# Kernel tuning notes

Measured on AMD Instinct MI355X. Metric: run time of the kernel, lower is better.

Reference implementation:

```python
import jax, jax.numpy as jnp
import numpy as np

B = 16          # graphs in batch
N = 10000       # original-graph nodes per graph
EG = 20000      # line-graph nodes (edges) per graph
E = B * EG      # total line-graph nodes
D = 384         # dim_inner
H = D // 3      # hdim
TOTAL_NODES = B * N


def setup_inputs() -> dict:
    key = jax.random.key(0)
    k1, k2 = jax.random.split(key)
    x = jax.random.normal(k1, (E, D), dtype=jnp.float32)
    org_graph_size = jnp.full((B,), N, dtype=jnp.int32)
    ptr = jnp.arange(B + 1, dtype=jnp.int32) * EG
    lg_node_idx = jax.random.randint(k2, (E, 2), 0, N, dtype=jnp.int32)
    return {"x": x, "org_graph_size": org_graph_size, "ptr": ptr, "lg_node_idx": lg_node_idx}


def _scatter_mean(x, idx, num_segments):
    # segment mean: sum / count (count clamped to 1 for empty segments)
    s = jax.ops.segment_sum(x, idx, num_segments=num_segments)
    c = jax.ops.segment_sum(jnp.ones((x.shape[0],), x.dtype), idx, num_segments=num_segments)
    return s / jnp.maximum(c, 1.0)[:, None]


def reference(x, org_graph_size, ptr, lg_node_idx):
    # per-graph node-index offsets (cumsum with leading zero, drop last)
    offsets = jnp.cumsum(
        jnp.concatenate([jnp.zeros((1,), org_graph_size.dtype), org_graph_size])
    )[:-1]
    # repeat each graph's offset for each of its line-graph nodes
    edge_counts = ptr[1:] - ptr[:-1]
    padding = jnp.repeat(offsets, edge_counts, total_repeat_length=E)
    idx = lg_node_idx + padding[:, None]  # [E, 2] global node indices

    outgoing = _scatter_mean(x, idx[:, 0], TOTAL_NODES)
    incoming = _scatter_mean(x, idx[:, 1], TOTAL_NODES)

    # lgvariant == 21
    return jnp.concatenate([incoming[:, : 2 * H], outgoing[:, 2 * H :]], axis=1)
```

## Files before the change

kernel.cpp:

```cpp
#include <hip/hip_runtime.h>

#define DIM 384
#define HALFC 256
#define C4PER 96

#define SCAN_BLOCK 256
#define SCAN_ITEMS 8
#define SCAN_CHUNK (SCAN_BLOCK * SCAN_ITEMS)

__global__ void count_kernel(const int* __restrict__ org, const int* __restrict__ ptr,
                             const int* __restrict__ lg, int B, int E, int TN,
                             int* __restrict__ cnt) {
    int e = blockIdx.x * blockDim.x + threadIdx.x;
    if (e >= E) return;
    int off = 0;
    for (int j = 0; j < B; ++j)
        if (e >= ptr[j + 1]) off += org[j];
    int n_out = lg[2 * e]     + off;
    int n_in  = lg[2 * e + 1] + off;
    atomicAdd(&cnt[n_in], 1);
    atomicAdd(&cnt[TN + n_out], 1);
}

__global__ void scan1_kernel(const int* __restrict__ cnt, int* __restrict__ offs,
                             int* __restrict__ bsum, int n) {
    __shared__ int s[SCAN_BLOCK];
    int base = blockIdx.x * SCAN_CHUNK;
    int tid = threadIdx.x;
    int v[SCAN_ITEMS];
    int tsum = 0;
#pragma unroll
    for (int j = 0; j < SCAN_ITEMS; ++j) {
        int i = base + tid * SCAN_ITEMS + j;
        v[j] = (i < n) ? cnt[i] : 0;
        tsum += v[j];
    }
    s[tid] = tsum;
    __syncthreads();
    for (int d = 1; d < SCAN_BLOCK; d <<= 1) {
        int t = (tid >= d) ? s[tid - d] : 0;
        __syncthreads();
        s[tid] += t;
        __syncthreads();
    }
    if (tid == SCAN_BLOCK - 1) bsum[blockIdx.x] = s[SCAN_BLOCK - 1];
    int run = (tid > 0) ? s[tid - 1] : 0;
#pragma unroll
    for (int j = 0; j < SCAN_ITEMS; ++j) {
        int i = base + tid * SCAN_ITEMS + j;
        if (i < n) offs[i] = run;
        run += v[j];
    }
}

__global__ void scan2_kernel(int* __restrict__ bsum, int nb) {
    __shared__ int s[SCAN_BLOCK];
    int tid = threadIdx.x;
    int carry = 0;
    for (int base = 0; base < nb; base += SCAN_BLOCK) {
        int i = base + tid;
        s[tid] = (i < nb) ? bsum[i] : 0;
        __syncthreads();
        for (int d = 1; d < SCAN_BLOCK; d <<= 1) {
            int t = (tid >= d) ? s[tid - d] : 0;
            __syncthreads();
            s[tid] += t;
            __syncthreads();
        }
        int excl = carry + ((tid > 0) ? s[tid - 1] : 0);
        if (i < nb) bsum[i] = excl;
        carry += s[SCAN_BLOCK - 1];
        __syncthreads();
    }
}

__global__ void scan3_kernel(int* __restrict__ offs, const int* __restrict__ bsum, int n) {
    int i = blockIdx.x * blockDim.x + threadIdx.x;
    if (i < n) offs[i] += bsum[i / SCAN_CHUNK];
}

__global__ void fill_kernel(const int* __restrict__ org, const int* __restrict__ ptr,
                            const int* __restrict__ lg, int B, int E, int TN,
                            int* __restrict__ offs, int* __restrict__ list) {
    int e = blockIdx.x * blockDim.x + threadIdx.x;
    if (e >= E) return;
    int off = 0;
    for (int j = 0; j < B; ++j)
        if (e >= ptr[j + 1]) off += org[j];
    int n_out = lg[2 * e]     + off;
    int n_in  = lg[2 * e + 1] + off;
    int p = atomicAdd(&offs[n_in], 1);
    list[p] = e;
    int q = atomicAdd(&offs[TN + n_out], 1);
    list[q] = e;
}

__global__ void gather_kernel(const float4* __restrict__ x4,
                              const int* __restrict__ cnt, const int* __restrict__ offs_end,
                              const int* __restrict__ list,
                              float4* __restrict__ out4, int TN, int total) {
    int i = blockIdx.x * blockDim.x + threadIdx.x;
    if (i >= total) return;
    int node = i / C4PER;
    int c4 = i - node * C4PER;
    int slot = (c4 * 4 < HALFC) ? node : TN + node;
    int deg = cnt[slot];
    int end = offs_end[slot];
    int start = end - deg;
    float4 acc = {0.f, 0.f, 0.f, 0.f};
    for (int k = start; k < end; ++k) {
        int e = list[k];
        float4 v = x4[(long)e * C4PER + c4];
        acc.x += v.x; acc.y += v.y; acc.z += v.z; acc.w += v.w;
    }
    float inv = 1.0f / (float)max(deg, 1);
    acc.x *= inv; acc.y *= inv; acc.z *= inv; acc.w *= inv;
    out4[i] = acc;
}

extern "C" void kernel_launch(void* const* d_in, const int* in_sizes, int n_in,
                              void* d_out, int out_size, void* d_ws, size_t ws_size,
                              hipStream_t stream) {
    const float* x = (const float*)d_in[0];
    const int* org = (const int*)d_in[1];
    const int* ptr = (const int*)d_in[2];
    const int* lg  = (const int*)d_in[3];

    int B  = in_sizes[1];
    int E  = in_sizes[3] / 2;
    int TN = out_size / DIM;
    int n2 = 2 * TN;

    int* cnt  = (int*)d_ws;
    int* offs = cnt + n2;
    int* bsum = offs + n2;
    int* list = bsum + 1024;

    hipMemsetAsync(cnt, 0, (size_t)n2 * sizeof(int), stream);

    count_kernel<<<(E + 255) / 256, 256, 0, stream>>>(org, ptr, lg, B, E, TN, cnt);

    int nb = (n2 + SCAN_CHUNK - 1) / SCAN_CHUNK;
    scan1_kernel<<<nb, SCAN_BLOCK, 0, stream>>>(cnt, offs, bsum, n2);
    scan2_kernel<<<1, SCAN_BLOCK, 0, stream>>>(bsum, nb);
    scan3_kernel<<<(n2 + 255) / 256, 256, 0, stream>>>(offs, bsum, n2);

    fill_kernel<<<(E + 255) / 256, 256, 0, stream>>>(org, ptr, lg, B, E, TN, offs, list);

    int total = TN * C4PER;
    gather_kernel<<<(total + 255) / 256, 256, 0, stream>>>((const float4*)x, cnt, offs, list,
                                                           (float4*)d_out, TN, total);
}
```

Baseline: 802.8 us.

## Record atomic ranks in count pass, drop fill atomics, split gather by half

The count kernel now saves the rank each atomicAdd returns per edge. The fill kernel uses those ranks with the scanned offsets to write list entries directly, with no second round of atomics. The gather kernel remaps threads so each warp covers only the incoming or only the outgoing column range, unrolls the neighbor loop by two, and adds launch bounds. The cost is an extra int2-per-edge workspace buffer, written and then read back.

```diff
diff --git a/kernel.cpp b/kernel.cpp
--- a/kernel.cpp
+++ b/kernel.cpp
@@ -1,7 +1,6 @@
 #include <hip/hip_runtime.h>
 
 #define DIM 384
-#define HALFC 256
 #define C4PER 96
 
 #define SCAN_BLOCK 256
@@ -9,17 +8,19 @@
 #define SCAN_CHUNK (SCAN_BLOCK * SCAN_ITEMS)
 
 __global__ void count_kernel(const int* __restrict__ org, const int* __restrict__ ptr,
-                             const int* __restrict__ lg, int B, int E, int TN,
-                             int* __restrict__ cnt) {
+                             const int2* __restrict__ lg2, int B, int E, int TN,
+                             int* __restrict__ cnt, int2* __restrict__ rk) {
     int e = blockIdx.x * blockDim.x + threadIdx.x;
     if (e >= E) return;
     int off = 0;
     for (int j = 0; j < B; ++j)
         if (e >= ptr[j + 1]) off += org[j];
-    int n_out = lg[2 * e]     + off;
-    int n_in  = lg[2 * e + 1] + off;
-    atomicAdd(&cnt[n_in], 1);
-    atomicAdd(&cnt[TN + n_out], 1);
+    int2 nn = lg2[e];
+    int n_out = nn.x + off;
+    int n_in  = nn.y + off;
+    int r_in  = atomicAdd(&cnt[n_in], 1);
+    int r_out = atomicAdd(&cnt[TN + n_out], 1);
+    rk[e] = make_int2(r_out, r_in);
 }
 
 __global__ void scan1_kernel(const int* __restrict__ cnt, int* __restrict__ offs,
@@ -80,42 +81,62 @@
 }
 
 __global__ void fill_kernel(const int* __restrict__ org, const int* __restrict__ ptr,
-                            const int* __restrict__ lg, int B, int E, int TN,
-                            int* __restrict__ offs, int* __restrict__ list) {
+                            const int2* __restrict__ lg2, const int2* __restrict__ rk,
+                            const int* __restrict__ offs, int B, int E, int TN,
+                            int* __restrict__ list) {
     int e = blockIdx.x * blockDim.x + threadIdx.x;
     if (e >= E) return;
     int off = 0;
     for (int j = 0; j < B; ++j)
         if (e >= ptr[j + 1]) off += org[j];
-    int n_out = lg[2 * e]     + off;
-    int n_in  = lg[2 * e + 1] + off;
-    int p = atomicAdd(&offs[n_in], 1);
-    list[p] = e;
-    int q = atomicAdd(&offs[TN + n_out], 1);
-    list[q] = e;
+    int2 nn = lg2[e];
+    int2 r  = rk[e];
+    list[offs[nn.y + off] + r.y] = e;
+    list[offs[TN + nn.x + off] + r.x] = e;
 }
 
-__global__ void gather_kernel(const float4* __restrict__ x4,
-                              const int* __restrict__ cnt, const int* __restrict__ offs_end,
-                              const int* __restrict__ list,
-                              float4* __restrict__ out4, int TN, int total) {
+__global__ __launch_bounds__(256, 8)
+void gather_kernel(const float4* __restrict__ x4,
+                   const int* __restrict__ cnt, const int* __restrict__ offs,
+                   const int* __restrict__ list,
+                   float4* __restrict__ out4, int TN) {
     int i = blockIdx.x * blockDim.x + threadIdx.x;
-    if (i >= total) return;
-    int node = i / C4PER;
-    int c4 = i - node * C4PER;
-    int slot = (c4 * 4 < HALFC) ? node : TN + node;
+    int tn64 = TN << 6;
+    int node, c4, slot;
+    if (i < tn64) {
+        node = i >> 6;
+        c4 = i & 63;
+        slot = node;
+    } else {
+        int j = i - tn64;
+        if (j >= (TN << 5)) return;
+        node = j >> 5;
+        c4 = 64 + (j & 31);
+        slot = TN + node;
+    }
+    int start = offs[slot];
     int deg = cnt[slot];
-    int end = offs_end[slot];
-    int start = end - deg;
-    float4 acc = {0.f, 0.f, 0.f, 0.f};
-    for (int k = start; k < end; ++k) {
-        int e = list[k];
-        float4 v = x4[(long)e * C4PER + c4];
-        acc.x += v.x; acc.y += v.y; acc.z += v.z; acc.w += v.w;
+    int end = start + deg;
+    float4 acc = make_float4(0.f, 0.f, 0.f, 0.f);
+    int k = start;
+    for (; k + 1 < end; k += 2) {
+        int e0 = list[k];
+        int e1 = list[k + 1];
+        float4 v0 = x4[e0 * C4PER + c4];
+        float4 v1 = x4[e1 * C4PER + c4];
+        acc.x += v0.x + v1.x;
+        acc.y += v0.y + v1.y;
+        acc.z += v0.z + v1.z;
+        acc.w += v0.w + v1.w;
+    }
+    if (k < end) {
+        int e0 = list[k];
+        float4 v0 = x4[e0 * C4PER + c4];
+        acc.x += v0.x; acc.y += v0.y; acc.z += v0.z; acc.w += v0.w;
     }
     float inv = 1.0f / (float)max(deg, 1);
     acc.x *= inv; acc.y *= inv; acc.z *= inv; acc.w *= inv;
-    out4[i] = acc;
+    out4[node * C4PER + c4] = acc;
 }
 
 extern "C" void kernel_launch(void* const* d_in, const int* in_sizes, int n_in,
@@ -135,19 +156,22 @@
     int* offs = cnt + n2;
     int* bsum = offs + n2;
     int* list = bsum + 1024;
+    int2* rk  = (int2*)(list + 2 * E);
 
     hipMemsetAsync(cnt, 0, (size_t)n2 * sizeof(int), stream);
 
-    count_kernel<<<(E + 255) / 256, 256, 0, stream>>>(org, ptr, lg, B, E, TN, cnt);
+    count_kernel<<<(E + 255) / 256, 256, 0, stream>>>(org, ptr, (const int2*)lg, B, E, TN,
+                                                      cnt, rk);
 
     int nb = (n2 + SCAN_CHUNK - 1) / SCAN_CHUNK;
     scan1_kernel<<<nb, SCAN_BLOCK, 0, stream>>>(cnt, offs, bsum, n2);
     scan2_kernel<<<1, SCAN_BLOCK, 0, stream>>>(bsum, nb);
     scan3_kernel<<<(n2 + 255) / 256, 256, 0, stream>>>(offs, bsum, n2);
 
-    fill_kernel<<<(E + 255) / 256, 256, 0, stream>>>(org, ptr, lg, B, E, TN, offs, list);
+    fill_kernel<<<(E + 255) / 256, 256, 0, stream>>>(org, ptr, (const int2*)lg, rk, offs,
+                                                     B, E, TN, list);
 
     int total = TN * C4PER;
     gather_kernel<<<(total + 255) / 256, 256, 0, stream>>>((const float4*)x, cnt, offs, list,
-                                                           (float4*)d_out, TN, total);
+                                                           (float4*)d_out, TN);
 }
```

Measured after the change: 759.8 us. 5.4% less time.
